# Kernel tuning notes

Hardware: AMD Instinct MI355X
Metric: run time of the kernel (lower is better)

Reference implementation:

```python
import jax, jax.numpy as jnp
import numpy as np

N, C, D, T, V = 64, 64, 64, 300, 25  # batch, in_ch, out_ch, time, joints
EPS = 1e-5

def _shift(c, sign):
    i = np.arange(V)[:, None]
    j = np.arange(c)[None, :]
    return jnp.asarray(((i * c + j + sign * j * c) % (c * V)).reshape(-1).astype(np.int32))

def hardswish(x):
    return x * jnp.clip(x + 3.0, 0.0, 6.0) * (1.0 / 6.0)

def bn3(x, g, b):
    # BatchNorm1d on (n, ch, L): stats over (batch, length), training-mode batch stats
    m = x.mean((0, 2), keepdims=True)
    v = x.var((0, 2), keepdims=True)
    return g[None, :, None] * (x - m) * jax.lax.rsqrt(v + EPS) + b[None, :, None]

def setup_inputs():
    key = jax.random.key(0)
    ks = jax.random.split(key, 8)
    r = lambda k, s, sc=0.05: jax.random.normal(k, s, jnp.float32) * sc
    return {
        'x0': jax.random.normal(ks[0], (N, C, T, V), jnp.float32),
        'shift_in': _shift(C, +1),
        'shift_out': _shift(D, -1),
        'Wv': r(ks[1], (1, V)), 'bv': jnp.zeros((1,), jnp.float32),
        'gv': jnp.ones((1,), jnp.float32), 'bev': jnp.zeros((1,), jnp.float32),
        'Wt': r(ks[2], (1, T)), 'bt': jnp.zeros((1,), jnp.float32),
        'gt': jnp.ones((1,), jnp.float32), 'bet': jnp.zeros((1,), jnp.float32),
        'Ws': r(ks[3], (D, C)), 'bs': jnp.zeros((D,), jnp.float32),
        'gs': jnp.ones((D,), jnp.float32), 'bes': jnp.zeros((D,), jnp.float32),
        'Wv2': r(ks[4], (C, D)), 'bv2': jnp.zeros((C,), jnp.float32),
        'Wt2': r(ks[5], (D, D)), 'bt2': jnp.zeros((D,), jnp.float32),
        'Lw': r(ks[6], (C, D), (1.0 / D) ** 0.5), 'Lb': jnp.zeros((1, 1, D), jnp.float32),
        'gbn': jnp.ones((V * D,), jnp.float32), 'bbn': jnp.zeros((V * D,), jnp.float32),
    }

def _forward(x0, Wv, bv, gv, bev, Wt, bt, gt, bet, Ws, bs, gs, bes,
             Wv2, bv2, Wt2, bt2, Lw, Lb, gbn, bbn, shift_in, shift_out):
    n, c, t, v = x0.shape
    d = Lw.shape[1]
    # shift-in gather over flattened (v*c) columns
    x = x0.transpose(0, 2, 3, 1).reshape(n * t, v * c)[:, shift_in]
    x = x.reshape(n, t, v, c).transpose(0, 3, 1, 2)  # (n,c,t,v)
    # --- YczAtt ---
    xv = x.transpose(0, 3, 1, 2).reshape(n, v, c * t)        # (n,v,c*t)
    xv = hardswish(bn3(jnp.einsum('ov,nvl->nol', Wv, xv) + bv[:, None], gv, bev))
    xt = x.transpose(0, 2, 1, 3).reshape(n, t, c * v)        # (n,t,c*v)
    xt = hardswish(bn3(jnp.einsum('ot,ntl->nol', Wt, xt) + bt[:, None], gt, bet))
    xs = jnp.concatenate([xt, xv], axis=2).reshape(n, c, t + v)
    xs = hardswish(bn3(jnp.einsum('oc,ncl->nol', Ws, xs) + bs[:, None], gs, bes))
    x_time = xs[:, :, :t]                                    # (n,d,t)
    x_view = xs[:, :, t:]                                    # (n,d,v)
    x_time = (jnp.einsum('od,ndl->nol', Wt2, x_time) + bt2[:, None]).mean(0, keepdims=True)
    x_view = (jnp.einsum('cd,ndl->ncl', Wv2, x_view) + bv2[:, None]).mean(0, keepdims=True)
    x_time = jax.nn.sigmoid(x_time)                          # (1,d,t)
    x_view = jax.nn.sigmoid(x_view).transpose(0, 2, 1)       # (1,v,c)
    # --- gate + linear + shift-out + BN + residual ---
    xm = x.transpose(0, 2, 3, 1).reshape(n * t, v, c)
    xm = xm * (jnp.tanh(x_view) + 1.0)
    y = jnp.einsum('nwc,cd->nwd', xm, Lw) + Lb               # (n*t,v,d)
    y = y.reshape(n * t, v * d)[:, shift_out]
    m = y.mean(0)
    var = y.var(0)
    y = gbn * (y - m) * jax.lax.rsqrt(var + EPS) + bbn
    y = y.reshape(n, t, v, d).transpose(0, 3, 1, 2)          # (n,d,t,v)
    y = jax.nn.relu(y + x0)                                  # down = identity (c == d)
    return y, x_time

def reference(x0, shift_in, shift_out, Wv, bv, gv, bev, Wt, bt, gt, bet,
              Ws, bs, gs, bes, Wv2, bv2, Wt2, bt2, Lw, Lb, gbn, bbn):
    return _forward(x0, Wv, bv, gv, bev, Wt, bt, gt, bet, Ws, bs, gs, bes,
                    Wv2, bv2, Wt2, bt2, Lw, Lb, gbn, bbn, shift_in, shift_out)
```

## Files before the change

### kernel.cpp

```cpp
#include <hip/hip_runtime.h>

typedef unsigned short u16;
typedef unsigned int   u32;

#define EPSF 1e-5f

typedef __attribute__((ext_vector_type(8))) short bf16x8;
typedef __attribute__((ext_vector_type(4))) float f32x4;

__device__ __forceinline__ u16 f2us(float f){
  union { float f; u32 i; } v; v.f = f;
  u32 i = v.i;
  return (u16)((i + 0x7FFFu + ((i >> 16) & 1u)) >> 16);
}
__device__ __forceinline__ float us2f(u16 u){
  union { u32 i; float f; } v; v.i = ((u32)u) << 16; return v.f;
}
__device__ __forceinline__ float hswish(float x){
  return x * fminf(fmaxf(x + 3.f, 0.f), 6.f) * (1.f/6.f);
}
__device__ __forceinline__ float sigm(float x){ return 1.f / (1.f + expf(-x)); }

#define WS_PARTIAL 0
#define WS_XV      0
#define WS_XT      1228800
#define WS_XS      1331200
#define WS_S       2662400
#define WS_GATE    2683200
#define WS_PART1   2684800
#define WS_ACCXS   2685056
#define WS_COLSTAT 2685184
#define WS_ABN     2688384
#define WS_BBN     2689984
#define WS_YWS     2692096

__global__ __launch_bounds__(256) void k_zero(float* p, int cnt){
  int i = blockIdx.x*256 + threadIdx.x;
  if (i < cnt) p[i] = 0.f;
}

__global__ __launch_bounds__(256) void k1(const float* __restrict__ x0,
    const float* __restrict__ Wv, const float* __restrict__ bv,
    const float* __restrict__ Wt, const float* __restrict__ bt,
    float* __restrict__ ws)
{
  __shared__ float slab[7500];
  __shared__ float wvc[25];
  __shared__ float wts[300];
  __shared__ float colS[25];
  __shared__ float red[8];
  int blk = blockIdx.x;
  int c = blk & 63;
  int tid = threadIdx.x;
  const float4* src = (const float4*)(x0) + blk*1875;
  float4* dst = (float4*)slab;
  for (int i = tid; i < 1875; i += 256) dst[i] = src[i];
  int cm = c % 25;
  if (tid < 25){ wvc[tid] = Wv[(tid - cm + 25) % 25]; colS[tid] = 0.f; }
  for (int i = tid; i < 300; i += 256) wts[i] = Wt[i];
  __syncthreads();
  float bvf = bv[0];
  float s1 = 0.f, s2 = 0.f;
  float ca[25];
  #pragma unroll
  for (int u = 0; u < 25; u++) ca[u] = 0.f;
  for (int t = tid; t < 300; t += 256){
    const float* row = &slab[t*25];
    float wt = wts[t];
    float xv = bvf;
    #pragma unroll
    for (int u = 0; u < 25; u++){
      float xf = row[u];
      xv += wvc[u] * xf;
      ca[u] += wt * xf;
    }
    ws[WS_XV + blk*300 + t] = xv;
    s1 += xv; s2 += xv*xv;
  }
  #pragma unroll
  for (int off = 32; off >= 1; off >>= 1){
    s1 += __shfl_xor(s1, off);
    s2 += __shfl_xor(s2, off);
    #pragma unroll
    for (int u = 0; u < 25; u++) ca[u] += __shfl_xor(ca[u], off);
  }
  int lane = tid & 63, wvi = tid >> 6;
  if (lane == 0){
    #pragma unroll
    for (int u = 0; u < 25; u++) atomicAdd(&colS[u], ca[u]);
    red[wvi] = s1; red[4 + wvi] = s2;
  }
  __syncthreads();
  if (wvi == 0){
    float btf = bt[0];
    float val = 0.f;
    if (lane < 25){
      val = colS[(lane + cm) % 25] + btf;
      ws[WS_XT + blk*25 + lane] = val;
    }
    float t1 = val, t2 = val*val;
    #pragma unroll
    for (int off = 32; off >= 1; off >>= 1){ t1 += __shfl_xor(t1, off); t2 += __shfl_xor(t2, off); }
    if (lane == 0){
      float* slot = &ws[WS_PART1 + (blk & 63)*4];
      atomicAdd(slot+0, red[0]+red[1]+red[2]+red[3]);
      atomicAdd(slot+1, red[4]+red[5]+red[6]+red[7]);
      atomicAdd(slot+2, t1);
      atomicAdd(slot+3, t2);
    }
  }
}

__global__ __launch_bounds__(256) void k2(
    const float* __restrict__ Ws_, const float* __restrict__ gv, const float* __restrict__ bev,
    const float* __restrict__ gt, const float* __restrict__ bet,
    float* __restrict__ ws)
{
  __shared__ float xsc[64*82];
  __shared__ float wsl[64*65];
  __shared__ float accs[128];
  __shared__ float bnp[4];
  int tid = threadIdx.x;
  int n = blockIdx.x >> 2;
  int chunk = blockIdx.x & 3;
  int l0 = chunk * 82;
  int cw = (325 - l0 < 82) ? (325 - l0) : 82;
  if (tid < 64){
    float p0 = ws[WS_PART1 + tid*4 + 0];
    float p1 = ws[WS_PART1 + tid*4 + 1];
    float p2 = ws[WS_PART1 + tid*4 + 2];
    float p3 = ws[WS_PART1 + tid*4 + 3];
    #pragma unroll
    for (int off = 32; off >= 1; off >>= 1){
      p0 += __shfl_xor(p0, off); p1 += __shfl_xor(p1, off);
      p2 += __shfl_xor(p2, off); p3 += __shfl_xor(p3, off);
    }
    if (tid == 0){
      float Mv = 1228800.f;
      float mv = p0 / Mv;
      float varv = p1 / Mv - mv*mv;
      float av = gv[0] * rsqrtf(varv + EPSF);
      bnp[0] = av; bnp[1] = bev[0] - mv*av;
      float Mt = 102400.f;
      float mt = p2 / Mt;
      float vart = p3 / Mt - mt*mt;
      float at = gt[0] * rsqrtf(vart + EPSF);
      bnp[2] = at; bnp[3] = bet[0] - mt*at;
    }
  }
  for (int i = tid; i < 4096; i += 256){
    int o = i >> 6, cc = i & 63;
    wsl[o*65 + cc] = Ws_[i];
  }
  if (tid < 128) accs[tid] = 0.f;
  __syncthreads();
  float a_v = bnp[0], b_v = bnp[1], a_t = bnp[2], b_t = bnp[3];
  for (int i = tid; i < 64*cw; i += 256){
    int ch = i / cw, li = i - ch*cw;
    int f = ch*325 + l0 + li;
    float e;
    if (f < 1600) e = ws[WS_XT + n*1600 + f] * a_t + b_t;
    else          e = ws[WS_XV + n*19200 + (f - 1600)] * a_v + b_v;
    xsc[ch*82 + li] = hswish(e);
  }
  __syncthreads();
  int o = tid & 63;
  float s1 = 0.f, s2 = 0.f;
  for (int i = tid; i < 64*cw; i += 256){
    int li = i >> 6;
    float acc = 0.f;
    #pragma unroll 8
    for (int cc = 0; cc < 64; cc++)
      acc += wsl[o*65 + cc] * xsc[cc*82 + li];
    ws[WS_XS + (n*64 + o)*325 + l0 + li] = acc;
    s1 += acc; s2 += acc*acc;
  }
  atomicAdd(&accs[o*2+0], s1);
  atomicAdd(&accs[o*2+1], s2);
  __syncthreads();
  if (tid < 128) atomicAdd(&ws[WS_ACCXS + tid], accs[tid]);
}

__global__ __launch_bounds__(256) void k3(const float* __restrict__ gs, const float* __restrict__ bes,
                                          float* __restrict__ ws)
{
  int i = blockIdx.x*256 + threadIdx.x;
  if (i >= 20800) return;
  int dch = i / 325, l = i - dch*325;
  float s1 = ws[WS_ACCXS + dch*2], s2 = ws[WS_ACCXS + dch*2 + 1];
  float m = s1 / 20800.f;
  float var = s2 / 20800.f - m*m;
  float a = gs[dch] * rsqrtf(var + EPSF);
  float b = bes[dch] - m*a;
  float sum = 0.f;
  int n0 = blockIdx.y * 8;
  for (int n = n0; n < n0 + 8; n++)
    sum += hswish(ws[WS_XS + (n*64 + dch)*325 + l] * a + b);
  atomicAdd(&ws[WS_S + i], sum);
}

__global__ __launch_bounds__(256) void k4(const float* __restrict__ Wt2, const float* __restrict__ bt2,
    const float* __restrict__ Wv2, const float* __restrict__ bv2,
    float* __restrict__ out2, float* __restrict__ ws)
{
  int i = blockIdx.x*256 + threadIdx.x;
  if (i < 19200){
    int o = i / 300, t = i - o*300;
    float acc = 0.f;
    #pragma unroll 8
    for (int dd = 0; dd < 64; dd++)
      acc += Wt2[o*64+dd] * ws[WS_S + dd*325 + t];
    out2[i] = sigm(acc * (1.f/64.f) + bt2[o]);
  } else if (i < 20800){
    int g = i - 19200;
    int v = g >> 6, cc = g & 63;
    float acc = 0.f;
    #pragma unroll 8
    for (int dd = 0; dd < 64; dd++)
      acc += Wv2[cc*64+dd] * ws[WS_S + dd*325 + 300 + v];
    ws[WS_GATE + v*64 + cc] = tanhf(sigm(acc * (1.f/64.f) + bv2[cc])) + 1.f;
  }
}

__global__ __launch_bounds__(512, 2) void k5y(const float* __restrict__ x0,
    const float* __restrict__ Lw, float* __restrict__ ws, const int storeY)
{
  __shared__ u16 xraw[64*154];
  __shared__ u16 zsh[160*72];
  __shared__ u16 lwt[64*72];
  __shared__ float gate[1600];
  __shared__ float colacc[3300];
  int tid = threadIdx.x;
  int n = blockIdx.x >> 3, e8 = blockIdx.x & 7;
  int c0 = (e8*50) >> 3, c1 = ((e8+1)*50) >> 3;
  const float2* xsrc = (const float2*)x0;
  u32* yws = (u32*)(ws + WS_YWS);

  for (int i = tid; i < 1600; i += 512) gate[i] = ws[WS_GATE + i];
  for (int i = tid; i < 4096; i += 512){
    int c = i >> 6, d = i & 63;
    lwt[d*72 + c] = f2us(Lw[c*64 + d]);
  }
  for (int i = tid; i < 3300; i += 512) colacc[i] = 0.f;
  for (int i = tid; i < 640; i += 512){ int c = i & 63, r = 150 + (i >> 6); zsh[r*72 + c] = 0; }
  for (int i = tid; i < 4800; i += 512){
    int c = i / 75, j = i - c*75;
    float2 xy = xsrc[(n*64 + c)*3750 + c0*75 + j];
    *(u32*)&xraw[c*154 + 2*j] = (u32)f2us(xy.x) | ((u32)f2us(xy.y) << 16);
  }

  u32 gsrc[10]; int gadr[10];
  #pragma unroll
  for (int k = 0; k < 10; k++){
    int p = tid + k*512;
    if (k < 9 || p < 4800){
      int cp = (p & 31)*2, r = p >> 5;
      int v = r - 25*((r*41) >> 10);
      int base = r - v;
      int w = v + cp;
      int u1 = w - 25*((w*41) >> 10);
      int w2 = w + 1;
      int u2 = w2 - 25*((w2*41) >> 10);
      gsrc[k] = (u32)(cp*154 + base + u1) | ((u32)((cp+1)*154 + base + u2) << 16);
      gadr[k] = v*64 + cp;
    }
  }

  int lane = tid & 63, wvi = tid >> 6;
  int m16 = lane & 15, kq = lane >> 4;
  int dd = (wvi & 3)*16 + m16;

  u32 eidx[20];
  #pragma unroll
  for (int it = 0; it < 5; it++){
    int T = wvi + it*8;
    int r0 = (T >> 2) * 16;
    #pragma unroll
    for (int q = 0; q < 4; q++){
      int r = r0 + kq*4 + q;
      u32 e = 0xFFFFu;
      if (r < 150){
        int v = r - 25*((r*41) >> 10);
        int w = v + dd;
        int u = w - 25*((w*41) >> 10);
        e = (u32)(dd*154 + (r - v) + u);
      }
      eidx[it*4 + q] = e;
    }
  }

  bf16x8 b0, b1;
  float s_acc[20], q_acc[20];
  #pragma unroll
  for (int z = 0; z < 20; z++){ s_acc[z] = 0.f; q_acc[z] = 0.f; }

  for (int cc = c0; cc < c1; cc++){
    __syncthreads();
    #pragma unroll
    for (int k = 0; k < 10; k++){
      if (k < 9 || tid < 192){
        int p = tid + k*512;
        int dst = (p >> 5)*72 + (p & 31)*2;
        float gA = gate[gadr[k]];
        float gB = gate[gadr[k] + 1];
        u16 x1 = xraw[gsrc[k] & 0xFFFFu];
        u16 x2 = xraw[gsrc[k] >> 16];
        u32 pk = (u32)f2us(us2f(x1)*gA) | ((u32)f2us(us2f(x2)*gB) << 16);
        *(u32*)&zsh[dst] = pk;
      }
    }
    __syncthreads();
    if (cc == c0){
      b0 = *(const bf16x8*)&lwt[dd*72 + kq*8];
      b1 = *(const bf16x8*)&lwt[dd*72 + 32 + kq*8];
    }
    float2 pf[10];
    bool has = (cc + 1 < c1);
    if (has){
      #pragma unroll
      for (int k = 0; k < 10; k++){
        int i = tid + k*512;
        if (i < 4800){
          int c = i / 75, j = i - c*75;
          pf[k] = xsrc[(n*64 + c)*3750 + (cc+1)*75 + j];
        }
      }
    }
    f32x4 acc[5];
    #pragma unroll
    for (int it = 0; it < 5; it++){
      int T = wvi + it*8;
      int r0 = (T >> 2) * 16;
      bf16x8 a0 = *(const bf16x8*)&zsh[(r0 + m16)*72 + kq*8];
      bf16x8 a1 = *(const bf16x8*)&zsh[(r0 + m16)*72 + 32 + kq*8];
      f32x4 a = {0.f,0.f,0.f,0.f};
      a = __builtin_amdgcn_mfma_f32_16x16x32_bf16(a0, b0, a, 0, 0, 0);
      a = __builtin_amdgcn_mfma_f32_16x16x32_bf16(a1, b1, a, 0, 0, 0);
      acc[it] = a;
      #pragma unroll
      for (int q = 0; q < 4; q++){
        float y = a[q];
        s_acc[it*4 + q] += y;
        q_acc[it*4 + q] += y*y;
      }
    }
    if (storeY){
      #pragma unroll
      for (int s = 0; s < 20; s++){
        u32 e = eidx[s];
        if (e != 0xFFFFu) xraw[e] = f2us(acc[s>>2][s&3]);
      }
      __syncthreads();
      for (int i = tid; i < 4800; i += 512){
        int d = i / 75, j = i - d*75;
        yws[(n*64 + d)*3750 + cc*75 + j] = *(const u32*)&xraw[d*154 + 2*j];
      }
    }
    __syncthreads();
    if (has){
      #pragma unroll
      for (int k = 0; k < 10; k++){
        int i = tid + k*512;
        if (i < 4800){
          int c = i / 75, j = i - c*75;
          *(u32*)&xraw[c*154 + 2*j] = (u32)f2us(pf[k].x) | ((u32)f2us(pf[k].y) << 16);
        }
      }
    }
  }
  #pragma unroll
  for (int it = 0; it < 5; it++){
    int T = wvi + it*8;
    int r0 = (T >> 2) * 16;
    #pragma unroll
    for (int q = 0; q < 4; q++){
      int r = r0 + kq*4 + q;
      if (r < 150){
        int v = r - 25*((r*41) >> 10);
        atomicAdd(&colacc[v*66 + dd], s_acc[it*4 + q]);
        atomicAdd(&colacc[1650 + v*66 + dd], q_acc[it*4 + q]);
      }
    }
  }
  __syncthreads();
  float* dst = ws + WS_PARTIAL + blockIdx.x*3200;
  for (int i = tid; i < 3200; i += 512){
    int f = (i < 1600) ? i : (i - 1600);
    int v = f >> 6, d = f & 63;
    dst[i] = colacc[((i < 1600) ? 0 : 1650) + v*66 + d];
  }
}

__global__ __launch_bounds__(256) void k5a(float* __restrict__ ws)
{
  __shared__ float red[256];
  int tid = threadIdx.x;
  int f = blockIdx.x*64 + (tid & 63);
  int bsub = tid >> 6;
  const float* src = ws + WS_PARTIAL + f;
  float acc = 0.f;
  #pragma unroll 8
  for (int b = bsub; b < 512; b += 4)
    acc += src[b*3200];
  red[tid] = acc;
  __syncthreads();
  if (tid < 64){
    float t = red[tid] + red[tid+64] + red[tid+128] + red[tid+192];
    ws[WS_COLSTAT + f] = t;
  }
}

__global__ __launch_bounds__(256) void k5b(const float* __restrict__ gbn, const float* __restrict__ bbn,
                                           float* __restrict__ ws, const int rot)
{
  int i = blockIdx.x*256 + threadIdx.x;
  if (i >= 1600) return;
  int v = i >> 6, d = i & 63;
  float s = ws[WS_COLSTAT + i], q = ws[WS_COLSTAT + 1600 + i];
  float m = s / 19200.f;
  float var = q / 19200.f - m*m;
  float rs = rsqrtf(var + EPSF);
  int vi = (v + d) % 25;
  int f = vi*64 + d;
  float a = gbn[f] * rs;
  int o = rot ? (vi*64 + d) : i;
  ws[WS_ABN + o] = a;
  ws[WS_BBN + o] = bbn[f] - m*a;
}

__global__ __launch_bounds__(256) void k6n(const float* __restrict__ x0,
    float* __restrict__ out, const float* __restrict__ ws)
{
  __shared__ float sA[25];
  __shared__ float sB[25];
  int row = blockIdx.x;
  int d = row & 63;
  int tid = threadIdx.x;
  if (tid < 25)       sA[tid]      = ws[WS_ABN + tid*64 + d];
  else if (tid < 50)  sB[tid - 25] = ws[WS_BBN + (tid - 25)*64 + d];
  __syncthreads();
  const u32*    yrow = (const u32*)(ws + WS_YWS) + row*3750;
  const float2* xrow = (const float2*)x0 + row*3750;
  float2*       orow = (float2*)out + row*3750;
  for (int j = tid; j < 3750; j += 256){
    u32 pk = yrow[j];
    float2 xv = xrow[j];
    int u0 = (2*j) % 25;
    int u1 = (u0 == 24) ? 0 : (u0 + 1);
    float2 o;
    o.x = fmaxf(us2f((u16)(pk & 0xFFFFu)) * sA[u0] + sB[u0] + xv.x, 0.f);
    o.y = fmaxf(us2f((u16)(pk >> 16))     * sA[u1] + sB[u1] + xv.y, 0.f);
    orow[j] = o;
  }
}

__global__ __launch_bounds__(512, 2) void k6(const float* __restrict__ x0,
    const float* __restrict__ Lw, float* __restrict__ out, float* __restrict__ ws)
{
  __shared__ u16 xraw[64*154];
  __shared__ u16 zsh[160*72];
  __shared__ u16 lwt[64*72];
  __shared__ float gate[1600];
  __shared__ float affA[1650];
  __shared__ float affB[1650];
  int tid = threadIdx.x;
  int n = blockIdx.x >> 3, e8 = blockIdx.x & 7;
  int c0 = (e8*50) >> 3, c1 = ((e8+1)*50) >> 3;
  const float2* xsrc = (const float2*)x0;

  for (int i = tid; i < 1600; i += 512){
    gate[i] = ws[WS_GATE + i];
    int v = i >> 6, d = i & 63;
    affA[v*66 + d] = ws[WS_ABN + i];
    affB[v*66 + d] = ws[WS_BBN + i];
  }
  for (int i = tid; i < 4096; i += 512){
    int c = i >> 6, d = i & 63;
    lwt[d*72 + c] = f2us(Lw[c*64 + d]);
  }
  for (int i = tid; i < 640; i += 512){ int c = i & 63, r = 150 + (i >> 6); zsh[r*72 + c] = 0; }
  for (int i = tid; i < 4800; i += 512){
    int c = i / 75, j = i - c*75;
    float2 xy = xsrc[(n*64 + c)*3750 + c0*75 + j];
    *(u32*)&xraw[c*154 + 2*j] = (u32)f2us(xy.x) | ((u32)f2us(xy.y) << 16);
  }

  u32 gsrc[10]; int gadr[10];
  #pragma unroll
  for (int k = 0; k < 10; k++){
    int p = tid + k*512;
    if (k < 9 || p < 4800){
      int cp = (p & 31)*2, r = p >> 5;
      int v = r - 25*((r*41) >> 10);
      int base = r - v;
      int w = v + cp;
      int u1 = w - 25*((w*41) >> 10);
      int w2 = w + 1;
      int u2 = w2 - 25*((w2*41) >> 10);
      gsrc[k] = (u32)(cp*154 + base + u1) | ((u32)((cp+1)*154 + base + u2) << 16);
      gadr[k] = v*64 + cp;
    }
  }

  int lane = tid & 63, wvi = tid >> 6;
  int m16 = lane & 15, kq = lane >> 4;
  int dd = (wvi & 3)*16 + m16;

  u32 eidx[20];
  #pragma unroll
  for (int it = 0; it < 5; it++){
    int T = wvi + it*8;
    int r0 = (T >> 2) * 16;
    #pragma unroll
    for (int q = 0; q < 4; q++){
      int r = r0 + kq*4 + q;
      u32 e = 0xFFFFu;
      if (r < 150){
        int v = r - 25*((r*41) >> 10);
        int w = v + dd;
        int u = w - 25*((w*41) >> 10);
        e = (u32)(dd*154 + (r - v) + u) | ((u32)(v*66 + dd) << 16);
      }
      eidx[it*4 + q] = e;
    }
  }

  bf16x8 b0, b1;

  for (int cc = c0; cc < c1; cc++){
    __syncthreads();
    #pragma unroll
    for (int k = 0; k < 10; k++){
      if (k < 9 || tid < 192){
        int p = tid + k*512;
        int dst = (p >> 5)*72 + (p & 31)*2;
        float gA = gate[gadr[k]];
        float gB = gate[gadr[k] + 1];
        u16 x1 = xraw[gsrc[k] & 0xFFFFu];
        u16 x2 = xraw[gsrc[k] >> 16];
        u32 pk = (u32)f2us(us2f(x1)*gA) | ((u32)f2us(us2f(x2)*gB) << 16);
        *(u32*)&zsh[dst] = pk;
      }
    }
    __syncthreads();
    if (cc == c0){
      b0 = *(const bf16x8*)&lwt[dd*72 + kq*8];
      b1 = *(const bf16x8*)&lwt[dd*72 + 32 + kq*8];
    }
    float2 pf[10];
    bool has = (cc + 1 < c1);
    if (has){
      #pragma unroll
      for (int k = 0; k < 10; k++){
        int i = tid + k*512;
        if (i < 4800){
          int c = i / 75, j = i - c*75;
          pf[k] = xsrc[(n*64 + c)*3750 + (cc+1)*75 + j];
        }
      }
    }
    f32x4 acc[5];
    #pragma unroll
    for (int it = 0; it < 5; it++){
      int T = wvi + it*8;
      int r0 = (T >> 2) * 16;
      bf16x8 a0 = *(const bf16x8*)&zsh[(r0 + m16)*72 + kq*8];
      bf16x8 a1 = *(const bf16x8*)&zsh[(r0 + m16)*72 + 32 + kq*8];
      f32x4 a = {0.f,0.f,0.f,0.f};
      a = __builtin_amdgcn_mfma_f32_16x16x32_bf16(a0, b0, a, 0, 0, 0);
      a = __builtin_amdgcn_mfma_f32_16x16x32_bf16(a1, b1, a, 0, 0, 0);
      acc[it] = a;
    }
    #pragma unroll
    for (int s = 0; s < 20; s++){
      u32 e = eidx[s];
      if ((e & 0xFFFFu) != 0xFFFFu){
        int idx = (int)(e & 0xFFFFu), ao = (int)(e >> 16);
        float resid = us2f(xraw[idx]);
        float val = acc[s>>2][s&3] * affA[ao] + affB[ao] + resid;
        xraw[idx] = f2us(fmaxf(val, 0.f));
      }
    }
    __syncthreads();
    for (int i = tid; i < 4800; i += 512){
      int d = i / 75, j = i - d*75;
      u32 pk = *(const u32*)&xraw[d*154 + 2*j];
      float2 o; o.x = us2f((u16)(pk & 0xFFFFu)); o.y = us2f((u16)(pk >> 16));
      ((float2*)out)[(n*64 + d)*3750 + cc*75 + j] = o;
    }
    __syncthreads();
    if (has){
      #pragma unroll
      for (int k = 0; k < 10; k++){
        int i = tid + k*512;
        if (i < 4800){
          int c = i / 75, j = i - c*75;
          *(u32*)&xraw[c*154 + 2*j] = (u32)f2us(pf[k].x) | ((u32)f2us(pf[k].y) << 16);
        }
      }
    }
  }
}

extern "C" void kernel_launch(void* const* d_in, const int* in_sizes, int n_in,
                              void* d_out, int out_size, void* d_ws, size_t ws_size,
                              hipStream_t stream)
{
  const float* x0  = (const float*)d_in[0];
  const float* Wv  = (const float*)d_in[3];
  const float* bv  = (const float*)d_in[4];
  const float* gv  = (const float*)d_in[5];
  const float* bev = (const float*)d_in[6];
  const float* Wt  = (const float*)d_in[7];
  const float* bt  = (const float*)d_in[8];
  const float* gt  = (const float*)d_in[9];
  const float* bet = (const float*)d_in[10];
  const float* Ws_ = (const float*)d_in[11];
  const float* gs  = (const float*)d_in[13];
  const float* bes = (const float*)d_in[14];
  const float* Wv2 = (const float*)d_in[15];
  const float* bv2 = (const float*)d_in[16];
  const float* Wt2 = (const float*)d_in[17];
  const float* bt2 = (const float*)d_in[18];
  const float* Lw  = (const float*)d_in[19];
  const float* gbn = (const float*)d_in[21];
  const float* bbn = (const float*)d_in[22];
  float* out = (float*)d_out;
  float* ws = (float*)d_ws;

  const int big = (ws_size >= (size_t)(WS_YWS + 15360000) * 4) ? 1 : 0;

  k_zero<<<dim3(14), dim3(256), 0, stream>>>(ws + WS_PART1, 3584);
  k_zero<<<dim3(82), dim3(256), 0, stream>>>(ws + WS_S, 20800);
  k1<<<dim3(4096), dim3(256), 0, stream>>>(x0, Wv, bv, Wt, bt, ws);
  k2<<<dim3(256), dim3(256), 0, stream>>>(Ws_, gv, bev, gt, bet, ws);
  k3<<<dim3(82, 8), dim3(256), 0, stream>>>(gs, bes, ws);
  k4<<<dim3(82), dim3(256), 0, stream>>>(Wt2, bt2, Wv2, bv2, out + 30720000, ws);
  k5y<<<dim3(512), dim3(512), 0, stream>>>(x0, Lw, ws, big);
  k5a<<<dim3(50), dim3(256), 0, stream>>>(ws);
  k5b<<<dim3(7), dim3(256), 0, stream>>>(gbn, bbn, ws, big);
  if (big){
    k6n<<<dim3(4096), dim3(256), 0, stream>>>(x0, out, ws);
  } else {
    k6<<<dim3(512), dim3(512), 0, stream>>>(x0, Lw, out, ws);
  }
}
```

Baseline: 488.6 us.

## Replace atomic reductions with per-block partials and fuse small stat kernels

Removes the two zeroing kernels by writing per-block partial sums to workspace slots instead of accumulating them atomically, then reduces those slots inside the consuming kernels (k2, k34). It fuses k3 and k4 into a single 13-block kernel that computes the pooled hardswish sums and both gate projections, and fuses k5a and k5b into one kernel. The final elementwise kernel is widened to float4 loads and stores. This cuts launch count and global atomics, but k34 runs on only 13 blocks that each loop serially over the batch, which may be slow.

Result: slower. 578.0 us (+18.3%).

```diff
diff --git a/kernel.cpp b/kernel.cpp
--- a/kernel.cpp
+++ b/kernel.cpp
@@ -25,19 +25,12 @@
 #define WS_XV      0
 #define WS_XT      1228800
 #define WS_XS      1331200
-#define WS_S       2662400
 #define WS_GATE    2683200
-#define WS_PART1   2684800
-#define WS_ACCXS   2685056
-#define WS_COLSTAT 2685184
 #define WS_ABN     2688384
 #define WS_BBN     2689984
-#define WS_YWS     2692096
-
-__global__ __launch_bounds__(256) void k_zero(float* p, int cnt){
-  int i = blockIdx.x*256 + threadIdx.x;
-  if (i < cnt) p[i] = 0.f;
-}
+#define WS_P1B     2692096
+#define WS_A2B     2708480
+#define WS_YWS     2741248
 
 __global__ __launch_bounds__(256) void k1(const float* __restrict__ x0,
     const float* __restrict__ Wv, const float* __restrict__ bv,
@@ -102,11 +95,11 @@
     #pragma unroll
     for (int off = 32; off >= 1; off >>= 1){ t1 += __shfl_xor(t1, off); t2 += __shfl_xor(t2, off); }
     if (lane == 0){
-      float* slot = &ws[WS_PART1 + (blk & 63)*4];
-      atomicAdd(slot+0, red[0]+red[1]+red[2]+red[3]);
-      atomicAdd(slot+1, red[4]+red[5]+red[6]+red[7]);
-      atomicAdd(slot+2, t1);
-      atomicAdd(slot+3, t2);
+      float4 pv;
+      pv.x = red[0]+red[1]+red[2]+red[3];
+      pv.y = red[4]+red[5]+red[6]+red[7];
+      pv.z = t1; pv.w = t2;
+      *(float4*)&ws[WS_P1B + blk*4] = pv;
     }
   }
 }
@@ -120,39 +113,49 @@
   __shared__ float wsl[64*65];
   __shared__ float accs[128];
   __shared__ float bnp[4];
+  __shared__ float pr[4][4];
   int tid = threadIdx.x;
   int n = blockIdx.x >> 2;
   int chunk = blockIdx.x & 3;
   int l0 = chunk * 82;
   int cw = (325 - l0 < 82) ? (325 - l0) : 82;
-  if (tid < 64){
-    float p0 = ws[WS_PART1 + tid*4 + 0];
-    float p1 = ws[WS_PART1 + tid*4 + 1];
-    float p2 = ws[WS_PART1 + tid*4 + 2];
-    float p3 = ws[WS_PART1 + tid*4 + 3];
+  {
+    float4 acc = {0.f,0.f,0.f,0.f};
+    const float4* p4 = (const float4*)&ws[WS_P1B];
+    for (int b = tid; b < 4096; b += 256){
+      float4 v = p4[b];
+      acc.x += v.x; acc.y += v.y; acc.z += v.z; acc.w += v.w;
+    }
     #pragma unroll
     for (int off = 32; off >= 1; off >>= 1){
-      p0 += __shfl_xor(p0, off); p1 += __shfl_xor(p1, off);
-      p2 += __shfl_xor(p2, off); p3 += __shfl_xor(p3, off);
-    }
-    if (tid == 0){
-      float Mv = 1228800.f;
-      float mv = p0 / Mv;
-      float varv = p1 / Mv - mv*mv;
-      float av = gv[0] * rsqrtf(varv + EPSF);
-      bnp[0] = av; bnp[1] = bev[0] - mv*av;
-      float Mt = 102400.f;
-      float mt = p2 / Mt;
-      float vart = p3 / Mt - mt*mt;
-      float at = gt[0] * rsqrtf(vart + EPSF);
-      bnp[2] = at; bnp[3] = bet[0] - mt*at;
-    }
+      acc.x += __shfl_xor(acc.x, off); acc.y += __shfl_xor(acc.y, off);
+      acc.z += __shfl_xor(acc.z, off); acc.w += __shfl_xor(acc.w, off);
+    }
+    int lane = tid & 63, wv = tid >> 6;
+    if (lane == 0){ pr[wv][0] = acc.x; pr[wv][1] = acc.y; pr[wv][2] = acc.z; pr[wv][3] = acc.w; }
   }
   for (int i = tid; i < 4096; i += 256){
     int o = i >> 6, cc = i & 63;
     wsl[o*65 + cc] = Ws_[i];
   }
   if (tid < 128) accs[tid] = 0.f;
+  __syncthreads();
+  if (tid == 0){
+    float p0 = pr[0][0]+pr[1][0]+pr[2][0]+pr[3][0];
+    float p1 = pr[0][1]+pr[1][1]+pr[2][1]+pr[3][1];
+    float p2 = pr[0][2]+pr[1][2]+pr[2][2]+pr[3][2];
+    float p3 = pr[0][3]+pr[1][3]+pr[2][3]+pr[3][3];
+    float Mv = 1228800.f;
+    float mv = p0 / Mv;
+    float varv = p1 / Mv - mv*mv;
+    float av = gv[0] * rsqrtf(varv + EPSF);
+    bnp[0] = av; bnp[1] = bev[0] - mv*av;
+    float Mt = 102400.f;
+    float mt = p2 / Mt;
+    float vart = p3 / Mt - mt*mt;
+    float at = gt[0] * rsqrtf(vart + EPSF);
+    bnp[2] = at; bnp[3] = bet[0] - mt*at;
+  }
   __syncthreads();
   float a_v = bnp[0], b_v = bnp[1], a_t = bnp[2], b_t = bnp[3];
   for (int i = tid; i < 64*cw; i += 256){
@@ -178,47 +181,76 @@
   atomicAdd(&accs[o*2+0], s1);
   atomicAdd(&accs[o*2+1], s2);
   __syncthreads();
-  if (tid < 128) atomicAdd(&ws[WS_ACCXS + tid], accs[tid]);
-}
-
-__global__ __launch_bounds__(256) void k3(const float* __restrict__ gs, const float* __restrict__ bes,
-                                          float* __restrict__ ws)
-{
-  int i = blockIdx.x*256 + threadIdx.x;
-  if (i >= 20800) return;
-  int dch = i / 325, l = i - dch*325;
-  float s1 = ws[WS_ACCXS + dch*2], s2 = ws[WS_ACCXS + dch*2 + 1];
-  float m = s1 / 20800.f;
-  float var = s2 / 20800.f - m*m;
-  float a = gs[dch] * rsqrtf(var + EPSF);
-  float b = bes[dch] - m*a;
-  float sum = 0.f;
-  int n0 = blockIdx.y * 8;
-  for (int n = n0; n < n0 + 8; n++)
-    sum += hswish(ws[WS_XS + (n*64 + dch)*325 + l] * a + b);
-  atomicAdd(&ws[WS_S + i], sum);
-}
-
-__global__ __launch_bounds__(256) void k4(const float* __restrict__ Wt2, const float* __restrict__ bt2,
+  if (tid < 128) ws[WS_A2B + blockIdx.x*128 + tid] = accs[tid];
+}
+
+__global__ __launch_bounds__(256) void k34(const float* __restrict__ gs, const float* __restrict__ bes,
+    const float* __restrict__ Wt2, const float* __restrict__ bt2,
     const float* __restrict__ Wv2, const float* __restrict__ bv2,
     float* __restrict__ out2, float* __restrict__ ws)
 {
-  int i = blockIdx.x*256 + threadIdx.x;
-  if (i < 19200){
-    int o = i / 300, t = i - o*300;
-    float acc = 0.f;
+  __shared__ float a2r[256];
+  __shared__ float w2[4096];
+  __shared__ float aS[64], bS[64];
+  __shared__ float Sl[64*26];
+  int tid = threadIdx.x;
+  bool isV = (blockIdx.x == 12);
+  int t0 = blockIdx.x * 25;
+  {
+    int j = tid & 127, h = tid >> 7;
+    float s = 0.f;
     #pragma unroll 8
-    for (int dd = 0; dd < 64; dd++)
-      acc += Wt2[o*64+dd] * ws[WS_S + dd*325 + t];
-    out2[i] = sigm(acc * (1.f/64.f) + bt2[o]);
-  } else if (i < 20800){
-    int g = i - 19200;
-    int v = g >> 6, cc = g & 63;
-    float acc = 0.f;
+    for (int b = h*128; b < h*128 + 128; ++b)
+      s += ws[WS_A2B + b*128 + j];
+    a2r[h*128 + j] = s;
+  }
+  const float* Wsel = isV ? Wv2 : Wt2;
+  for (int i = tid; i < 4096; i += 256) w2[i] = Wsel[i];
+  __syncthreads();
+  if (tid < 64){
+    float s1 = a2r[2*tid]   + a2r[128 + 2*tid];
+    float s2 = a2r[2*tid+1] + a2r[128 + 2*tid+1];
+    float m = s1 / 20800.f;
+    float var = s2 / 20800.f - m*m;
+    float a = gs[tid] * rsqrtf(var + EPSF);
+    aS[tid] = a; bS[tid] = bes[tid] - m*a;
+  }
+  __syncthreads();
+  int offk[7]; float ak[7], bk[7]; int dk_[7], tk_[7]; bool vk[7];
+  #pragma unroll
+  for (int k = 0; k < 7; k++){
+    int i = tid + 256*k;
+    vk[k] = (i < 1600);
+    if (vk[k]){
+      int dd = i / 25, tt = i - dd*25;
+      dk_[k] = dd; tk_[k] = tt;
+      offk[k] = dd*325 + (isV ? (300 + tt) : (t0 + tt));
+      ak[k] = aS[dd]; bk[k] = bS[dd];
+    }
+  }
+  float acc[7];
+  #pragma unroll
+  for (int k = 0; k < 7; k++) acc[k] = 0.f;
+  for (int n = 0; n < 64; ++n){
+    const float* base = ws + WS_XS + n*20800;
+    #pragma unroll
+    for (int k = 0; k < 7; k++)
+      if (vk[k]) acc[k] += hswish(ak[k]*base[offk[k]] + bk[k]);
+  }
+  #pragma unroll
+  for (int k = 0; k < 7; k++)
+    if (vk[k]) Sl[dk_[k]*26 + tk_[k]] = acc[k];
+  __syncthreads();
+  int o = tid & 63, tq = tid >> 6;
+  float bias = isV ? bv2[o] : bt2[o];
+  for (int tv = tq; tv < 25; tv += 4){
+    float s = 0.f;
     #pragma unroll 8
-    for (int dd = 0; dd < 64; dd++)
-      acc += Wv2[cc*64+dd] * ws[WS_S + dd*325 + 300 + v];
-    ws[WS_GATE + v*64 + cc] = tanhf(sigm(acc * (1.f/64.f) + bv2[cc])) + 1.f;
+    for (int d = 0; d < 64; ++d)
+      s += w2[o*64 + d] * Sl[d*26 + tv];
+    float val = sigm(s * (1.f/64.f) + bias);
+    if (isV) ws[WS_GATE + tv*64 + o] = tanhf(val) + 1.f;
+    else     out2[o*300 + t0 + tv] = val;
   }
 }
 
@@ -391,66 +423,67 @@
   }
 }
 
-__global__ __launch_bounds__(256) void k5a(float* __restrict__ ws)
-{
-  __shared__ float red[256];
+__global__ __launch_bounds__(256) void k5ab(const float* __restrict__ gbn, const float* __restrict__ bbn,
+                                            float* __restrict__ ws, const int rot)
+{
+  __shared__ float rs[4][64];
+  __shared__ float rq[4][64];
   int tid = threadIdx.x;
-  int f = blockIdx.x*64 + (tid & 63);
-  int bsub = tid >> 6;
-  const float* src = ws + WS_PARTIAL + f;
-  float acc = 0.f;
+  int fo = tid & 63, g = tid >> 6;
+  int f = blockIdx.x*64 + fo;
+  const float* src = ws + WS_PARTIAL;
+  float s = 0.f, q = 0.f;
   #pragma unroll 8
-  for (int b = bsub; b < 512; b += 4)
-    acc += src[b*3200];
-  red[tid] = acc;
+  for (int b = g*128; b < g*128 + 128; ++b){
+    s += src[b*3200 + f];
+    q += src[b*3200 + 1600 + f];
+  }
+  rs[g][fo] = s; rq[g][fo] = q;
   __syncthreads();
   if (tid < 64){
-    float t = red[tid] + red[tid+64] + red[tid+128] + red[tid+192];
-    ws[WS_COLSTAT + f] = t;
-  }
-}
-
-__global__ __launch_bounds__(256) void k5b(const float* __restrict__ gbn, const float* __restrict__ bbn,
-                                           float* __restrict__ ws, const int rot)
-{
-  int i = blockIdx.x*256 + threadIdx.x;
-  if (i >= 1600) return;
-  int v = i >> 6, d = i & 63;
-  float s = ws[WS_COLSTAT + i], q = ws[WS_COLSTAT + 1600 + i];
-  float m = s / 19200.f;
-  float var = q / 19200.f - m*m;
-  float rs = rsqrtf(var + EPSF);
-  int vi = (v + d) % 25;
-  int f = vi*64 + d;
-  float a = gbn[f] * rs;
-  int o = rot ? (vi*64 + d) : i;
-  ws[WS_ABN + o] = a;
-  ws[WS_BBN + o] = bbn[f] - m*a;
+    int d = tid, v = blockIdx.x;
+    float S = rs[0][d] + rs[1][d] + rs[2][d] + rs[3][d];
+    float Q = rq[0][d] + rq[1][d] + rq[2][d] + rq[3][d];
+    float m = S / 19200.f;
+    float var = Q / 19200.f - m*m;
+    float rsq = rsqrtf(var + EPSF);
+    int vi = (v + d) % 25;
+    int fi = vi*64 + d;
+    float a = gbn[fi] * rsq;
+    int o = rot ? (vi*64 + d) : (v*64 + d);
+    ws[WS_ABN + o] = a;
+    ws[WS_BBN + o] = bbn[fi] - m*a;
+  }
 }
 
 __global__ __launch_bounds__(256) void k6n(const float* __restrict__ x0,
     float* __restrict__ out, const float* __restrict__ ws)
 {
-  __shared__ float sA[25];
-  __shared__ float sB[25];
+  __shared__ float sA2[28];
+  __shared__ float sB2[28];
   int row = blockIdx.x;
   int d = row & 63;
   int tid = threadIdx.x;
-  if (tid < 25)       sA[tid]      = ws[WS_ABN + tid*64 + d];
-  else if (tid < 50)  sB[tid - 25] = ws[WS_BBN + (tid - 25)*64 + d];
-  __syncthreads();
-  const u32*    yrow = (const u32*)(ws + WS_YWS) + row*3750;
-  const float2* xrow = (const float2*)x0 + row*3750;
-  float2*       orow = (float2*)out + row*3750;
-  for (int j = tid; j < 3750; j += 256){
-    u32 pk = yrow[j];
-    float2 xv = xrow[j];
-    int u0 = (2*j) % 25;
-    int u1 = (u0 == 24) ? 0 : (u0 + 1);
-    float2 o;
-    o.x = fmaxf(us2f((u16)(pk & 0xFFFFu)) * sA[u0] + sB[u0] + xv.x, 0.f);
-    o.y = fmaxf(us2f((u16)(pk >> 16))     * sA[u1] + sB[u1] + xv.y, 0.f);
+  if (tid < 28){
+    int um = (tid >= 25) ? (tid - 25) : tid;
+    sA2[tid] = ws[WS_ABN + um*64 + d];
+    sB2[tid] = ws[WS_BBN + um*64 + d];
+  }
+  __syncthreads();
+  const uint2*  yrow = (const uint2*)((const u32*)(ws + WS_YWS) + row*3750);
+  const float4* xrow = (const float4*)x0 + row*1875;
+  float4*       orow = (float4*)out + row*1875;
+  int u = (4*tid) % 25;
+  for (int j = tid; j < 1875; j += 256){
+    uint2 yp = yrow[j];
+    float4 x = xrow[j];
+    float4 o;
+    o.x = fmaxf(us2f((u16)(yp.x & 0xFFFFu)) * sA2[u]   + sB2[u]   + x.x, 0.f);
+    o.y = fmaxf(us2f((u16)(yp.x >> 16))     * sA2[u+1] + sB2[u+1] + x.y, 0.f);
+    o.z = fmaxf(us2f((u16)(yp.y & 0xFFFFu)) * sA2[u+2] + sB2[u+2] + x.z, 0.f);
+    o.w = fmaxf(us2f((u16)(yp.y >> 16))     * sA2[u+3] + sB2[u+3] + x.w, 0.f);
     orow[j] = o;
+    u = (u == 0) ? 24 : (u - 1);
   }
 }
 
@@ -630,15 +663,11 @@
 
   const int big = (ws_size >= (size_t)(WS_YWS + 15360000) * 4) ? 1 : 0;
 
-  k_zero<<<dim3(14), dim3(256), 0, stream>>>(ws + WS_PART1, 3584);
-  k_zero<<<dim3(82), dim3(256), 0, stream>>>(ws + WS_S, 20800);
   k1<<<dim3(4096), dim3(256), 0, stream>>>(x0, Wv, bv, Wt, bt, ws);
   k2<<<dim3(256), dim3(256), 0, stream>>>(Ws_, gv, bev, gt, bet, ws);
-  k3<<<dim3(82, 8), dim3(256), 0, stream>>>(gs, bes, ws);
-  k4<<<dim3(82), dim3(256), 0, stream>>>(Wt2, bt2, Wv2, bv2, out + 30720000, ws);
+  k34<<<dim3(13), dim3(256), 0, stream>>>(gs, bes, Wt2, bt2, Wv2, bv2, out + 30720000, ws);
   k5y<<<dim3(512), dim3(512), 0, stream>>>(x0, Lw, ws, big);
-  k5a<<<dim3(50), dim3(256), 0, stream>>>(ws);
-  k5b<<<dim3(7), dim3(256), 0, stream>>>(gbn, bbn, ws, big);
+  k5ab<<<dim3(25), dim3(256), 0, stream>>>(gbn, bbn, ws, big);
   if (big){
     k6n<<<dim3(4096), dim3(256), 0, stream>>>(x0, out, ws);
   } else {
```
